# Performance work log

Measured on AMD Instinct MI355X. Metric: run time of the kernel, lower is better.

Reference implementation:

```python
import jax, jax.numpy as jnp
from jax import lax
import numpy as np

B, L, FEAT, EXTRA, K1 = 128, 128, 36, 12, 3
EMB, H, A, T_OUT = 6, 1024, 256, 24
CONV_OUT = FEAT - 2 * (K1 - 1)  # 32


def _conv1d(x, w):
    return lax.conv_general_dilated(x, w, (1,), 'VALID', dimension_numbers=('NCW', 'OIW', 'NCW'))


def _lstm(x_t, h, c, Wih, Whh, b):
    g = x_t @ Wih.T + h @ Whh.T + b
    i, f, gg, o = jnp.split(g, 4, axis=-1)
    c = jax.nn.sigmoid(f) * c + jax.nn.sigmoid(i) * jnp.tanh(gg)
    h = jax.nn.sigmoid(o) * jnp.tanh(c)
    return h, c


def setup_inputs():
    key = jax.random.key(0)
    ks = jax.random.split(key, 20)
    s = 0.05
    r = lambda k, sh: jax.random.normal(k, sh, jnp.float32) * s
    return {
        'x': jax.random.normal(ks[0], (B, L, FEAT + EXTRA), jnp.float32),
        'conv1_w': r(ks[1], (L, L, K1)), 'conv1_b': r(ks[2], (L,)),
        'conv2_w': r(ks[3], (L, L, K1)), 'conv2_b': r(ks[4], (L,)),
        'lin3_w': r(ks[5], (EMB, CONV_OUT)), 'lin3_b': r(ks[6], (EMB,)),
        'enc_Wih': r(ks[7], (4 * H, EMB + EXTRA)), 'enc_Whh': r(ks[8], (4 * H, H)), 'enc_b': r(ks[9], (4 * H,)),
        'attn_Wq': r(ks[10], (A, H)), 'attn_Wk': r(ks[11], (A, H)), 'attn_Wv': r(ks[12], (1, A)),
        'dec_Wih': r(ks[13], (4 * H, 2 * H)), 'dec_Whh': r(ks[14], (4 * H, H)), 'dec_b': r(ks[15], (4 * H,)),
        'out_w': r(ks[16], (1, H)), 'out_b': r(ks[17], (1,)),
    }


def reference(x, conv1_w, conv1_b, conv2_w, conv2_b, lin3_w, lin3_b,
              enc_Wih, enc_Whh, enc_b, attn_Wq, attn_Wk, attn_Wv,
              dec_Wih, dec_Whh, dec_b, out_w, out_b):
    # CNN feature extractor over the dense (short-interval) features
    dense = x[:, :, :FEAT]                                   # (B, L, 36)
    h1 = jax.nn.softplus(_conv1d(dense, conv1_w) + conv1_b[None, :, None])
    h2 = jax.nn.relu(_conv1d(h1, conv2_w) + conv2_b[None, :, None])  # (B, L, 32)
    lin = jnp.einsum('blf,ef->ble', h2, lin3_w) + lin3_b     # (B, L, EMB)
    lstm_in = jnp.concatenate([lin, x[:, :, FEAT:]], axis=2)  # (B, L, EMB+EXTRA)

    # LSTM encoder
    def enc_step(carry, xt):
        h, c = carry
        h, c = _lstm(xt, h, c, enc_Wih, enc_Whh, enc_b)
        return (h, c), h
    z = jnp.zeros((B, H), jnp.float32)
    (h, c), outs = lax.scan(enc_step, (z, z), lstm_in.transpose(1, 0, 2))
    enc_out = outs.transpose(1, 0, 2)                        # (B, L, H)
    s = enc_out[:, -1]

    # fixed-size key buffer; original appends s_t each step (lengths 128..151)
    M = L - 1 + T_OUT
    buf0 = jnp.zeros((B, M, H), jnp.float32).at[:, :L - 1].set(enc_out[:, :-1])
    pos = jnp.arange(M)

    def dec_step(carry, t):
        h, c, s, buf = carry
        buf = lax.dynamic_update_slice(buf, s[:, None, :], (0, L - 1 + t, 0))
        mask = (pos <= L - 1 + t).astype(buf.dtype)
        q = jnp.stack([h, c], axis=1)                        # (B, 2, H)
        qp = q @ attn_Wq.T                                   # (B, 2, A)
        kp = buf @ attn_Wk.T                                 # (B, M, A)
        feats = jnp.tanh(qp[:, :, None, :] + kp[:, None, :, :])  # (B, 2, M, A)
        scores = jnp.einsum('bnma,a->bnm', feats, attn_Wv[0])
        # original: softmax over dim=1 (query axis); mask keys post-softmax
        w = jax.nn.softmax(scores, axis=1) * mask[None, None, :]
        ctx = jnp.einsum('bnm,bmh->bnh', w, buf).reshape(B, 2 * H)
        h, c = _lstm(ctx, h, c, dec_Wih, dec_Whh, dec_b)
        y = (h @ out_w.T + out_b)[:, 0]
        return (h, c, h, buf), y

    _, ys = lax.scan(dec_step, (h, c, s, buf0), jnp.arange(T_OUT))
    return ys.T                                              # (B, T_OUT)
```

## Files before the change

kernel.cpp:

```cpp
#include <hip/hip_runtime.h>
#include <math.h>


#define NB 128
#define NL 128
#define NH 1024
#define NA 256
#define NT 24
#define NM 151

typedef __attribute__((ext_vector_type(8))) short bf16x8;
typedef __attribute__((ext_vector_type(8))) short s16x8;
typedef __attribute__((ext_vector_type(4))) float f32x4;

#define MFMA(a, b, acc) __builtin_amdgcn_mfma_f32_16x16x32_bf16(a, b, acc, 0, 0, 0)

#define I16_SCALE 32767.0f
#define I16_INV   (1.0f / 32767.0f)

__device__ __forceinline__ float sig_f(float x) {
  return 1.0f / (1.0f + __expf(-x));
}
__device__ __forceinline__ float tanh_f(float x) {
  x = fminf(9.0f, fmaxf(-9.0f, x));
  float e = __expf(2.0f * x);
  return (e - 1.0f) / (e + 1.0f);
}
__device__ __forceinline__ unsigned short f2bf(float f) {
  unsigned int u = __float_as_uint(f);
  u = (u + 0x7FFFu + ((u >> 16) & 1u)) >> 16;
  return (unsigned short)u;
}
__device__ __forceinline__ float bf2f(unsigned short u) {
  return __uint_as_float(((unsigned int)u) << 16);
}
__device__ __forceinline__ short f2i16(float f) {
  return (short)__float2int_rn(f * I16_SCALE);
}

__global__ __launch_bounds__(128) void conv_front(
    const float* __restrict__ x,
    const float* __restrict__ w1, const float* __restrict__ b1,
    const float* __restrict__ w2, const float* __restrict__ b2,
    const float* __restrict__ w3, const float* __restrict__ b3,
    float* __restrict__ lstm_in)
{
  int b = blockIdx.x;
  int t = threadIdx.x;
  __shared__ float d[128][36];
  __shared__ float h1[128][34];
  __shared__ float h2[128][32];

  const float* xr = x + (size_t)(b * NL + t) * 48;
  #pragma unroll
  for (int f = 0; f < 36; ++f) d[t][f] = xr[f];
  __syncthreads();

  float acc[34];
  {
    float bias = b1[t];
    #pragma unroll
    for (int w = 0; w < 34; ++w) acc[w] = bias;
  }
  const float* wr = w1 + t * 384;
  for (int ci = 0; ci < 128; ++ci) {
    float row[36];
    #pragma unroll
    for (int f = 0; f < 36; ++f) row[f] = d[ci][f];
    float wa = wr[ci * 3 + 0], wb = wr[ci * 3 + 1], wc = wr[ci * 3 + 2];
    #pragma unroll
    for (int w = 0; w < 34; ++w)
      acc[w] += row[w] * wa + row[w + 1] * wb + row[w + 2] * wc;
  }
  #pragma unroll
  for (int w = 0; w < 34; ++w) {
    float z = acc[w];
    h1[t][w] = (z > 20.0f) ? z : log1pf(__expf(z));
  }
  __syncthreads();

  float acc2[32];
  {
    float bias = b2[t];
    #pragma unroll
    for (int w = 0; w < 32; ++w) acc2[w] = bias;
  }
  const float* wr2 = w2 + t * 384;
  for (int ci = 0; ci < 128; ++ci) {
    float row[34];
    #pragma unroll
    for (int f = 0; f < 34; ++f) row[f] = h1[ci][f];
    float wa = wr2[ci * 3 + 0], wb = wr2[ci * 3 + 1], wc = wr2[ci * 3 + 2];
    #pragma unroll
    for (int w = 0; w < 32; ++w)
      acc2[w] += row[w] * wa + row[w + 1] * wb + row[w + 2] * wc;
  }
  #pragma unroll
  for (int w = 0; w < 32; ++w) h2[t][w] = fmaxf(acc2[w], 0.0f);
  __syncthreads();

  float* outr = lstm_in + (size_t)(b * NL + t) * 18;
  #pragma unroll
  for (int e = 0; e < 6; ++e) {
    float s = b3[e];
    #pragma unroll
    for (int f = 0; f < 32; ++f) s += h2[t][f] * w3[e * 32 + f];
    outr[e] = s;
  }
  #pragma unroll
  for (int j = 0; j < 12; ++j) outr[6 + j] = xr[36 + j];
}

__global__ void frag_w4(const float* __restrict__ src, int K, int kshift,
                        unsigned short* __restrict__ hi,
                        unsigned short* __restrict__ lo, int ngroups)
{
  int o = blockIdx.x * 256 + threadIdx.x;
  if (o >= ngroups) return;
  int lane = o & 63;
  int ki = (o >> 6) & ((1 << kshift) - 1);
  int t2 = o >> (6 + kshift);
  int l15 = lane & 15, q = lane >> 4;
  int grow = (l15 >> 2) * 1024 + t2 * 4 + (l15 & 3);
  const float* s = src + (size_t)grow * K + ki * 32 + q * 8;
  unsigned short hv[8], lv[8];
  #pragma unroll
  for (int j = 0; j < 8; ++j) {
    float v = s[j];
    hv[j] = f2bf(v);
    lv[j] = f2bf(v - bf2f(hv[j]));
  }
  size_t e = (size_t)o * 8;
  *(ushort4*)(hi + e) = make_ushort4(hv[0], hv[1], hv[2], hv[3]);
  *(ushort4*)(hi + e + 4) = make_ushort4(hv[4], hv[5], hv[6], hv[7]);
  *(ushort4*)(lo + e) = make_ushort4(lv[0], lv[1], lv[2], lv[3]);
  *(ushort4*)(lo + e + 4) = make_ushort4(lv[4], lv[5], lv[6], lv[7]);
}

__global__ void frag_wqk(const float* __restrict__ wq,
                         const float* __restrict__ wk,
                         unsigned short* __restrict__ hi,
                         unsigned short* __restrict__ lo)
{
  int o = blockIdx.x * 256 + threadIdx.x;
  if (o >= 65536) return;
  int lane = o & 63;
  int ki = (o >> 6) & 31;
  int ntile = o >> 11;
  int l15 = lane & 15, q = lane >> 4;
  int row = ntile * 16 + l15;
  int k = ki * 32 + q * 8;
  const float* s = (row < 256) ? (wq + (size_t)row * 1024 + k)
                               : (wk + (size_t)(row - 256) * 1024 + k);
  unsigned short hv[8], lv[8];
  #pragma unroll
  for (int j = 0; j < 8; ++j) {
    float v = s[j];
    hv[j] = f2bf(v);
    lv[j] = f2bf(v - bf2f(hv[j]));
  }
  size_t e = (size_t)o * 8;
  *(ushort4*)(hi + e) = make_ushort4(hv[0], hv[1], hv[2], hv[3]);
  *(ushort4*)(hi + e + 4) = make_ushort4(hv[4], hv[5], hv[6], hv[7]);
  *(ushort4*)(lo + e) = make_ushort4(lv[0], lv[1], lv[2], lv[3]);
  *(ushort4*)(lo + e + 4) = make_ushort4(lv[4], lv[5], lv[6], lv[7]);
}

__global__ void frag_wx4(const float* __restrict__ wih,
                         unsigned short* __restrict__ hi,
                         unsigned short* __restrict__ lo)
{
  int o = blockIdx.x * 256 + threadIdx.x;
  if (o >= 16384) return;
  int lane = o & 63;
  int t2 = o >> 6;
  int l15 = lane & 15, q = lane >> 4;
  int grow = (l15 >> 2) * 1024 + t2 * 4 + (l15 & 3);
  unsigned short hv[8], lv[8];
  #pragma unroll
  for (int j = 0; j < 8; ++j) {
    int k = q * 8 + j;
    float v = (k < 18) ? wih[(size_t)grow * 18 + k] : 0.0f;
    hv[j] = f2bf(v);
    lv[j] = f2bf(v - bf2f(hv[j]));
  }
  size_t e = (size_t)o * 8;
  *(ushort4*)(hi + e) = make_ushort4(hv[0], hv[1], hv[2], hv[3]);
  *(ushort4*)(hi + e + 4) = make_ushort4(hv[4], hv[5], hv[6], hv[7]);
  *(ushort4*)(lo + e) = make_ushort4(lv[0], lv[1], lv[2], lv[3]);
  *(ushort4*)(lo + e + 4) = make_ushort4(lv[4], lv[5], lv[6], lv[7]);
}

__global__ void frag_xs(const float* __restrict__ lstm_in,
                        unsigned short* __restrict__ hi,
                        unsigned short* __restrict__ lo)
{
  int o = blockIdx.x * 256 + threadIdx.x;
  if (o >= 65536) return;
  int lane = o & 63;
  int btile = (o >> 6) & 7;
  int t = o >> 9;
  int l15 = lane & 15, q = lane >> 4;
  int b = btile * 16 + l15;
  unsigned short hv[8], lv[8];
  #pragma unroll
  for (int j = 0; j < 8; ++j) {
    int k = q * 8 + j;
    float v = (k < 18) ? lstm_in[(size_t)(b * NL + t) * 18 + k] : 0.0f;
    hv[j] = f2bf(v);
    lv[j] = f2bf(v - bf2f(hv[j]));
  }
  size_t e = (size_t)o * 8;
  *(ushort4*)(hi + e) = make_ushort4(hv[0], hv[1], hv[2], hv[3]);
  *(ushort4*)(hi + e + 4) = make_ushort4(hv[4], hv[5], hv[6], hv[7]);
  *(ushort4*)(lo + e) = make_ushort4(lv[0], lv[1], lv[2], lv[3]);
  *(ushort4*)(lo + e + 4) = make_ushort4(lv[4], lv[5], lv[6], lv[7]);
}

__global__ void init_all(float* __restrict__ c,
                         unsigned short* __restrict__ hhi0,
                         unsigned short* __restrict__ hlo0,
                         float* __restrict__ out) {
  int i = blockIdx.x * 256 + threadIdx.x;
  if (i < NB * NH) { c[i] = 0.0f; hhi0[i] = 0; hlo0[i] = 0; }
  if (i < NB * NT) out[i] = 0.0f;
}

__global__ __launch_bounds__(512) void enc_step(
    const unsigned short* __restrict__ hfi_hi,
    const unsigned short* __restrict__ hfi_lo,
    unsigned short* __restrict__ hfo_hi,
    unsigned short* __restrict__ hfo_lo,
    const unsigned short* __restrict__ Wf_hi,
    const unsigned short* __restrict__ Wf_lo,
    const unsigned short* __restrict__ Wxf_hi,
    const unsigned short* __restrict__ Wxf_lo,
    const unsigned short* __restrict__ xsf_hi,
    const unsigned short* __restrict__ xsf_lo,
    const float* __restrict__ encb,
    float* __restrict__ c,
    short* __restrict__ buf,
    int t)
{
  __shared__ float G[2][128][17];
  int tid = threadIdx.x;
  int w8 = tid >> 6, lane = tid & 63;
  int grp = w8 >> 2, wm = w8 & 3;
  int l15 = lane & 15, q4 = (lane >> 4) * 4;
  int bx = blockIdx.x;

  const unsigned short* Bh = Wf_hi + (size_t)bx * 16384 + lane * 8;
  const unsigned short* Bl = Wf_lo + (size_t)bx * 16384 + lane * 8;
  const unsigned short* A0h = hfi_hi + (size_t)(2 * wm) * 512 + lane * 8;
  const unsigned short* A1h = hfi_hi + (size_t)(2 * wm + 1) * 512 + lane * 8;
  const unsigned short* A0l = hfi_lo + (size_t)(2 * wm) * 512 + lane * 8;
  const unsigned short* A1l = hfi_lo + (size_t)(2 * wm + 1) * 512 + lane * 8;

  f32x4 a00 = {0,0,0,0}, a10 = {0,0,0,0};
  for (int i = 0; i < 16; ++i) {
    int ki = grp * 16 + i;
    size_t ao = (size_t)ki * 4096;
    size_t bo = (size_t)ki * 512;
    bf16x8 x0h = *(const bf16x8*)(A0h + ao);
    bf16x8 x0l = *(const bf16x8*)(A0l + ao);
    bf16x8 x1h = *(const bf16x8*)(A1h + ao);
    bf16x8 x1l = *(const bf16x8*)(A1l + ao);
    bf16x8 yh = *(const bf16x8*)(Bh + bo);
    bf16x8 yl = *(const bf16x8*)(Bl + bo);
    a00 = MFMA(x0h, yh, a00); a00 = MFMA(x0l, yh, a00); a00 = MFMA(x0h, yl, a00);
    a10 = MFMA(x1h, yh, a10); a10 = MFMA(x1l, yh, a10); a10 = MFMA(x1h, yl, a10);
  }
  if (grp == 0) {
    size_t xo0 = ((size_t)t * 8 + 2 * wm) * 512 + lane * 8;
    size_t xo1 = xo0 + 512;
    bf16x8 x0h = *(const bf16x8*)(xsf_hi + xo0);
    bf16x8 x0l = *(const bf16x8*)(xsf_lo + xo0);
    bf16x8 x1h = *(const bf16x8*)(xsf_hi + xo1);
    bf16x8 x1l = *(const bf16x8*)(xsf_lo + xo1);
    size_t wo = (size_t)bx * 512 + lane * 8;
    bf16x8 yh = *(const bf16x8*)(Wxf_hi + wo);
    bf16x8 yl = *(const bf16x8*)(Wxf_lo + wo);
    a00 = MFMA(x0h, yh, a00); a00 = MFMA(x0l, yh, a00); a00 = MFMA(x0h, yl, a00);
    a10 = MFMA(x1h, yh, a10); a10 = MFMA(x1l, yh, a10); a10 = MFMA(x1h, yl, a10);
  }
  #pragma unroll
  for (int r = 0; r < 4; ++r) {
    G[grp][32 * wm + q4 + r][l15]      = a00[r];
    G[grp][32 * wm + 16 + q4 + r][l15] = a10[r];
  }
  __syncthreads();

  if (tid < 128) {
    int b = tid;
    int kc = bx * 4;
    float4 cold = *(const float4*)(c + (size_t)b * NH + kc);
    float rc[4], rh[4];
    #pragma unroll
    for (int j = 0; j < 4; ++j) {
      float gate[4];
      #pragma unroll
      for (int q = 0; q < 4; ++q) {
        int gi = q * 4 + j;
        gate[q] = G[0][b][gi] + G[1][b][gi] + encb[q * NH + kc + j];
      }
      float co = (&cold.x)[j];
      float cn = sig_f(gate[1]) * co + sig_f(gate[0]) * tanh_f(gate[2]);
      float hn = sig_f(gate[3]) * tanh_f(cn);
      rc[j] = cn; rh[j] = hn;
    }
    *(float4*)(c + (size_t)b * NH + kc) = make_float4(rc[0], rc[1], rc[2], rc[3]);
    unsigned short hh[4], hl[4];
    short hq[4];
    #pragma unroll
    for (int j = 0; j < 4; ++j) {
      hh[j] = f2bf(rh[j]);
      hl[j] = f2bf(rh[j] - bf2f(hh[j]));
      hq[j] = f2i16(rh[j]);
    }
    int ki = kc >> 5, qq = (kc >> 3) & 3, j8 = kc & 7;
    size_t fo = (size_t)ki * 4096 + (b >> 4) * 512 + ((b & 15) + 16 * qq) * 8 + j8;
    *(ushort4*)(hfo_hi + fo) = make_ushort4(hh[0], hh[1], hh[2], hh[3]);
    *(ushort4*)(hfo_lo + fo) = make_ushort4(hl[0], hl[1], hl[2], hl[3]);
    *(short4*)(buf + (size_t)(b * NM + t) * NH + kc) =
        make_short4(hq[0], hq[1], hq[2], hq[3]);
  }
}

__global__ __launch_bounds__(256) void dec_prep(
    const unsigned short* __restrict__ hf_hi,
    const unsigned short* __restrict__ hf_lo,
    const float* __restrict__ c,
    unsigned short* __restrict__ qhi, unsigned short* __restrict__ qlo)
{
  int b = blockIdx.x;
  int j4 = threadIdx.x * 4;
  int ki = j4 >> 5, qq = (j4 >> 3) & 3, j8 = j4 & 7;
  size_t fh = (size_t)ki * 4096 + (b >> 4) * 512 + ((b & 15) + 16 * qq) * 8 + j8;
  ushort4 hv = *(const ushort4*)(hf_hi + fh);
  ushort4 lv = *(const ushort4*)(hf_lo + fh);
  float4 cv = *(const float4*)(c + (size_t)b * NH + j4);
  unsigned short ch[4], cl[4];
  float cf[4] = {cv.x, cv.y, cv.z, cv.w};
  #pragma unroll
  for (int k = 0; k < 4; ++k) {
    ch[k] = f2bf(cf[k]); cl[k] = f2bf(cf[k] - bf2f(ch[k]));
  }
  int rt = (2 * b) >> 4;
  int rl = ((2 * b) & 15) + 16 * qq;
  size_t fq = (size_t)ki * 8192 + rt * 512 + rl * 8 + j8;
  *(ushort4*)(qhi + fq) = hv;
  *(ushort4*)(qlo + fq) = lv;
  *(ushort4*)(qhi + fq + 8) = make_ushort4(ch[0], ch[1], ch[2], ch[3]);
  *(ushort4*)(qlo + fq + 8) = make_ushort4(cl[0], cl[1], cl[2], cl[3]);
}

__global__ __launch_bounds__(128) void gemm_qk(
    const unsigned short* __restrict__ Ahi, const unsigned short* __restrict__ Alo,
    const unsigned short* __restrict__ Bhi, const unsigned short* __restrict__ Blo,
    float* __restrict__ C)
{
  int tid = threadIdx.x;
  int w = tid >> 6, lane = tid & 63;
  int l15 = lane & 15, q4 = (lane >> 4) * 4;
  int mtile = blockIdx.x;
  int ntile = blockIdx.y * 2 + w;

  const unsigned short* Ah = Ahi + (size_t)mtile * 512 + lane * 8;
  const unsigned short* Al = Alo + (size_t)mtile * 512 + lane * 8;
  const unsigned short* Bh = Bhi + (size_t)ntile * 16384 + lane * 8;
  const unsigned short* Bl = Blo + (size_t)ntile * 16384 + lane * 8;
  f32x4 acc = {0, 0, 0, 0};
  for (int ki = 0; ki < 32; ++ki) {
    size_t ao = (size_t)ki * 8192;
    size_t bo = (size_t)ki * 512;
    bf16x8 ah = *(const bf16x8*)(Ah + ao);
    bf16x8 al = *(const bf16x8*)(Al + ao);
    bf16x8 bh = *(const bf16x8*)(Bh + bo);
    bf16x8 bl = *(const bf16x8*)(Bl + bo);
    acc = MFMA(ah, bh, acc);
    acc = MFMA(al, bh, acc);
    acc = MFMA(ah, bl, acc);
  }
  #pragma unroll
  for (int r = 0; r < 4; ++r)
    C[(size_t)(mtile * 16 + q4 + r) * 512 + ntile * 16 + l15] = acc[r];
}

__global__ __launch_bounds__(256) void gemm_kp(
    const short* __restrict__ A,
    const unsigned short* __restrict__ Bhi,
    const unsigned short* __restrict__ Blo,
    unsigned short* __restrict__ C)
{
  int tid = threadIdx.x;
  int w = tid >> 6, lane = tid & 63;
  int l15 = lane & 15, q8 = (lane >> 4) * 8, q4 = (lane >> 4) * 4;
  size_t m0 = (size_t)blockIdx.x * 64;
  int n0 = blockIdx.y * 64 + w * 16;
  int ntile = 16 + blockIdx.y * 4 + w;

  const unsigned short* Bh = Bhi + (size_t)ntile * 16384 + lane * 8;
  const unsigned short* Bl = Blo + (size_t)ntile * 16384 + lane * 8;
  f32x4 acc[4] = {{0,0,0,0},{0,0,0,0},{0,0,0,0},{0,0,0,0}};
  for (int ki = 0; ki < 32; ++ki) {
    int ko = ki * 32 + q8;
    size_t bo = (size_t)ki * 512;
    bf16x8 bh = *(const bf16x8*)(Bh + bo);
    bf16x8 bl = *(const bf16x8*)(Bl + bo);
    #pragma unroll
    for (int i = 0; i < 4; ++i) {
      s16x8 av = *(const s16x8*)(A + (m0 + 16 * i + l15) * (size_t)NH + ko);
      bf16x8 ah;
      #pragma unroll
      for (int k = 0; k < 8; ++k)
        ah[k] = (short)f2bf((float)av[k] * I16_INV);
      acc[i] = MFMA(ah, bh, acc[i]);
      acc[i] = MFMA(ah, bl, acc[i]);
    }
  }
  #pragma unroll
  for (int i = 0; i < 4; ++i)
    #pragma unroll
    for (int r = 0; r < 4; ++r)
      C[(m0 + 16 * i + q4 + r) * NA + n0 + l15] = f2bf(acc[i][r]);
}

__global__ __launch_bounds__(256) void attn_kernel(
    const float* __restrict__ qkout,
    unsigned short* __restrict__ kp,
    const short* __restrict__ buf,
    const float* __restrict__ Wv,
    unsigned short* __restrict__ Xfhi,
    unsigned short* __restrict__ Xflo,
    int t)
{
  int b = blockIdx.x;
  int tid = threadIdx.x;
  int Mt = NL + t;
  __shared__ float sWv[256], q0[256], q1[256], kNew[256];
  __shared__ float sc[2][NM + 1];
  __shared__ float w0s[NM + 1], w1s[NM + 1];
  sWv[tid] = Wv[tid];
  q0[tid] = qkout[(size_t)(2 * b) * 512 + tid];
  q1[tid] = qkout[(size_t)(2 * b + 1) * 512 + tid];
  float kn = qkout[(size_t)(2 * b) * 512 + 256 + tid];
  kNew[tid] = kn;
  kp[((size_t)(b * NM) + (NL - 1 + t)) * NA + tid] = f2bf(kn);
  __syncthreads();

  for (int idx = tid; idx < 2 * Mt; idx += 256) {
    int m = idx >> 1, n = idx & 1;
    const float* q = n ? q1 : q0;
    float s = 0.0f;
    if (m == Mt - 1) {
      for (int a = 0; a < NA; ++a) s += tanh_f(q[a] + kNew[a]) * sWv[a];
    } else {
      const unsigned short* kpr = kp + ((size_t)(b * NM) + m) * NA;
      for (int a = 0; a < NA; a += 4) {
        ushort4 kv = *(const ushort4*)(kpr + a);
        s += tanh_f(q[a + 0] + bf2f(kv.x)) * sWv[a + 0];
        s += tanh_f(q[a + 1] + bf2f(kv.y)) * sWv[a + 1];
        s += tanh_f(q[a + 2] + bf2f(kv.z)) * sWv[a + 2];
        s += tanh_f(q[a + 3] + bf2f(kv.w)) * sWv[a + 3];
      }
    }
    sc[n][m] = s;
  }
  __syncthreads();
  for (int m = tid; m < Mt; m += 256) {
    float s0 = sc[0][m], s1 = sc[1][m];
    float mx = fmaxf(s0, s1);
    float e0 = __expf(s0 - mx), e1 = __expf(s1 - mx);
    float inv = 1.0f / (e0 + e1);
    w0s[m] = e0 * inv;
    w1s[m] = e1 * inv;
  }
  __syncthreads();

  float4 a0 = {0, 0, 0, 0}, a1 = {0, 0, 0, 0};
  const short* bb = buf + ((size_t)b * NM) * NH + tid * 4;
  for (int m = 0; m < Mt; ++m) {
    short4 v = *(const short4*)(bb + (size_t)m * NH);
    float vx = (float)v.x * I16_INV, vy = (float)v.y * I16_INV;
    float vz = (float)v.z * I16_INV, vw = (float)v.w * I16_INV;
    float w0 = w0s[m], w1 = w1s[m];
    a0.x += vx * w0; a0.y += vy * w0; a0.z += vz * w0; a0.w += vw * w0;
    a1.x += vx * w1; a1.y += vy * w1; a1.z += vz * w1; a1.w += vw * w1;
  }
  float v0[4] = {a0.x, a0.y, a0.z, a0.w};
  float v1[4] = {a1.x, a1.y, a1.z, a1.w};
  unsigned short h0[4], l0[4], h1v[4], l1v[4];
  #pragma unroll
  for (int k = 0; k < 4; ++k) {
    h0[k] = f2bf(v0[k]); l0[k] = f2bf(v0[k] - bf2f(h0[k]));
    h1v[k] = f2bf(v1[k]); l1v[k] = f2bf(v1[k] - bf2f(h1v[k]));
  }
  int k0 = tid * 4;
  size_t fo0 = (size_t)(k0 >> 5) * 4096 + (b >> 4) * 512 +
               ((b & 15) + 16 * ((k0 >> 3) & 3)) * 8 + (k0 & 7);
  int k1 = 1024 + tid * 4;
  size_t fo1 = (size_t)(k1 >> 5) * 4096 + (b >> 4) * 512 +
               ((b & 15) + 16 * ((k1 >> 3) & 3)) * 8 + (k1 & 7);
  *(ushort4*)(Xfhi + fo0) = make_ushort4(h0[0], h0[1], h0[2], h0[3]);
  *(ushort4*)(Xflo + fo0) = make_ushort4(l0[0], l0[1], l0[2], l0[3]);
  *(ushort4*)(Xfhi + fo1) = make_ushort4(h1v[0], h1v[1], h1v[2], h1v[3]);
  *(ushort4*)(Xflo + fo1) = make_ushort4(l1v[0], l1v[1], l1v[2], l1v[3]);
}

__global__ __launch_bounds__(512) void dec_step(
    const unsigned short* __restrict__ Xfhi,
    const unsigned short* __restrict__ Xflo,
    const unsigned short* __restrict__ qin_hi,
    const unsigned short* __restrict__ qin_lo,
    unsigned short* __restrict__ qout_hi,
    unsigned short* __restrict__ qout_lo,
    const unsigned short* __restrict__ Wdxf_hi,
    const unsigned short* __restrict__ Wdxf_lo,
    const unsigned short* __restrict__ Wdhf_hi,
    const unsigned short* __restrict__ Wdhf_lo,
    const float* __restrict__ decb,
    float* __restrict__ c,
    short* __restrict__ buf,
    const float* __restrict__ out_w, const float* __restrict__ out_b,
    float* __restrict__ out, int t)
{
  __shared__ float G[2][128][17];
  int tid = threadIdx.x;
  int w8 = tid >> 6, lane = tid & 63;
  int grp = w8 >> 2, wm = w8 & 3;
  int l15 = lane & 15, q4 = (lane >> 4) * 4;
  int bx = blockIdx.x;

  f32x4 a00 = {0,0,0,0}, a10 = {0,0,0,0};

  {
    const unsigned short* Wh = Wdxf_hi + (size_t)bx * 32768 + lane * 8;
    const unsigned short* Wl = Wdxf_lo + (size_t)bx * 32768 + lane * 8;
    const unsigned short* X0h = Xfhi + (size_t)(2 * wm) * 512 + lane * 8;
    const unsigned short* X1h = Xfhi + (size_t)(2 * wm + 1) * 512 + lane * 8;
    const unsigned short* X0l = Xflo + (size_t)(2 * wm) * 512 + lane * 8;
    const unsigned short* X1l = Xflo + (size_t)(2 * wm + 1) * 512 + lane * 8;
    int klo = grp ? 48 : 0;
    int khi = grp ? 64 : 48;
    for (int ki = klo; ki < khi; ++ki) {
      size_t ao = (size_t)ki * 4096;
      size_t bo = (size_t)ki * 512;
      bf16x8 x0h = *(const bf16x8*)(X0h + ao);
      bf16x8 x0l = *(const bf16x8*)(X0l + ao);
      bf16x8 x1h = *(const bf16x8*)(X1h + ao);
      bf16x8 x1l = *(const bf16x8*)(X1l + ao);
      bf16x8 yh = *(const bf16x8*)(Wh + bo);
      bf16x8 yl = *(const bf16x8*)(Wl + bo);
      a00 = MFMA(x0h, yh, a00); a00 = MFMA(x0l, yh, a00); a00 = MFMA(x0h, yl, a00);
      a10 = MFMA(x1h, yh, a10); a10 = MFMA(x1l, yh, a10); a10 = MFMA(x1h, yl, a10);
    }
  }
  if (grp) {
    int qt0 = 4 * wm + (l15 >> 3);
    int ln = 2 * (l15 & 7) + 16 * (lane >> 4);
    const unsigned short* A0h = qin_hi + (size_t)qt0 * 512 + ln * 8;
    const unsigned short* A0l = qin_lo + (size_t)qt0 * 512 + ln * 8;
    const unsigned short* A1h = qin_hi + (size_t)(qt0 + 2) * 512 + ln * 8;
    const unsigned short* A1l = qin_lo + (size_t)(qt0 + 2) * 512 + ln * 8;
    const unsigned short* Bh = Wdhf_hi + (size_t)bx * 16384 + lane * 8;
    const unsigned short* Bl = Wdhf_lo + (size_t)bx * 16384 + lane * 8;
    for (int ki = 0; ki < 32; ++ki) {
      size_t ao = (size_t)ki * 8192;
      size_t bo = (size_t)ki * 512;
      bf16x8 x0h = *(const bf16x8*)(A0h + ao);
      bf16x8 x0l = *(const bf16x8*)(A0l + ao);
      bf16x8 x1h = *(const bf16x8*)(A1h + ao);
      bf16x8 x1l = *(const bf16x8*)(A1l + ao);
      bf16x8 yh = *(const bf16x8*)(Bh + bo);
      bf16x8 yl = *(const bf16x8*)(Bl + bo);
      a00 = MFMA(x0h, yh, a00); a00 = MFMA(x0l, yh, a00); a00 = MFMA(x0h, yl, a00);
      a10 = MFMA(x1h, yh, a10); a10 = MFMA(x1l, yh, a10); a10 = MFMA(x1h, yl, a10);
    }
  }
  #pragma unroll
  for (int r = 0; r < 4; ++r) {
    G[grp][32 * wm + q4 + r][l15]      = a00[r];
    G[grp][32 * wm + 16 + q4 + r][l15] = a10[r];
  }
  __syncthreads();

  if (tid < 128) {
    int b = tid;
    int kc = bx * 4;
    float4 cold = *(const float4*)(c + (size_t)b * NH + kc);
    float rc[4], rh[4];
    #pragma unroll
    for (int j = 0; j < 4; ++j) {
      float gate[4];
      #pragma unroll
      for (int q = 0; q < 4; ++q) {
        int gi = q * 4 + j;
        gate[q] = G[0][b][gi] + G[1][b][gi] + decb[q * NH + kc + j];
      }
      float co = (&cold.x)[j];
      float cn = sig_f(gate[1]) * co + sig_f(gate[0]) * tanh_f(gate[2]);
      float hn = sig_f(gate[3]) * tanh_f(cn);
      rc[j] = cn; rh[j] = hn;
    }
    *(float4*)(c + (size_t)b * NH + kc) = make_float4(rc[0], rc[1], rc[2], rc[3]);

    float py = 0.0f;
    #pragma unroll
    for (int j = 0; j < 4; ++j) py += rh[j] * out_w[kc + j];
    if (bx == 0) py += out_b[0];
    atomicAdd(&out[b * NT + t], py);

    if (t < NT - 1) {
      unsigned short hh[4], hl[4], ch[4], cl[4];
      short hq[4];
      #pragma unroll
      for (int j = 0; j < 4; ++j) {
        hh[j] = f2bf(rh[j]); hl[j] = f2bf(rh[j] - bf2f(hh[j]));
        ch[j] = f2bf(rc[j]); cl[j] = f2bf(rc[j] - bf2f(ch[j]));
        hq[j] = f2i16(rh[j]);
      }
      *(short4*)(buf + (size_t)(b * NM + NL + t) * NH + kc) =
          make_short4(hq[0], hq[1], hq[2], hq[3]);
      int ki = kc >> 5, qq = (kc >> 3) & 3, j8 = kc & 7;
      int rt = (2 * b) >> 4;
      int rl = ((2 * b) & 15) + 16 * qq;
      size_t fq = (size_t)ki * 8192 + rt * 512 + rl * 8 + j8;
      *(ushort4*)(qout_hi + fq) = make_ushort4(hh[0], hh[1], hh[2], hh[3]);
      *(ushort4*)(qout_lo + fq) = make_ushort4(hl[0], hl[1], hl[2], hl[3]);
      *(ushort4*)(qout_hi + fq + 8) = make_ushort4(ch[0], ch[1], ch[2], ch[3]);
      *(ushort4*)(qout_lo + fq + 8) = make_ushort4(cl[0], cl[1], cl[2], cl[3]);
    }
  }
}

extern "C" void kernel_launch(void* const* d_in, const int* in_sizes, int n_in,
                              void* d_out, int out_size, void* d_ws, size_t ws_size,
                              hipStream_t stream) {
  const float* x       = (const float*)d_in[0];
  const float* conv1_w = (const float*)d_in[1];
  const float* conv1_b = (const float*)d_in[2];
  const float* conv2_w = (const float*)d_in[3];
  const float* conv2_b = (const float*)d_in[4];
  const float* lin3_w  = (const float*)d_in[5];
  const float* lin3_b  = (const float*)d_in[6];
  const float* enc_Wih = (const float*)d_in[7];
  const float* enc_Whh = (const float*)d_in[8];
  const float* enc_b   = (const float*)d_in[9];
  const float* attn_Wq = (const float*)d_in[10];
  const float* attn_Wk = (const float*)d_in[11];
  const float* attn_Wv = (const float*)d_in[12];
  const float* dec_Wih = (const float*)d_in[13];
  const float* dec_Whh = (const float*)d_in[14];
  const float* dec_b   = (const float*)d_in[15];
  const float* out_w   = (const float*)d_in[16];
  const float* out_b   = (const float*)d_in[17];
  float* out = (float*)d_out;

  unsigned short* W = (unsigned short*)d_ws;
  short*          buf    = (short*)W;
  unsigned short* kp     = W + (size_t)19791872;
  unsigned short* qA_hi  = kp + 4947968;
  unsigned short* qA_lo  = qA_hi + 262144;
  unsigned short* qB_hi  = qA_lo + 262144;
  unsigned short* qB_lo  = qB_hi + 262144;
  unsigned short* Xf_hi  = qB_lo + 262144;
  unsigned short* Xf_lo  = Xf_hi + 262144;
  unsigned short* Wqkf_hi = Xf_lo + 262144;
  unsigned short* Wqkf_lo = Wqkf_hi + 524288;
  unsigned short* Wdhf_hi = Wqkf_lo + 524288;
  unsigned short* Wdhf_lo = Wdhf_hi + 4194304;
  unsigned short* Wdxf_hi = Wdhf_lo + 4194304;
  unsigned short* Wdxf_lo = Wdxf_hi + 8388608;
  float* c     = (float*)(Wdxf_lo + 8388608);
  float* qkout = c + 131072;
  unsigned short* hfA_hi = Wdxf_hi;
  unsigned short* hfA_lo = Wdxf_hi + 131072;
  unsigned short* hfB_hi = Wdxf_hi + 262144;
  unsigned short* hfB_lo = Wdxf_hi + 393216;
  unsigned short* xsf_hi = Wdxf_hi + 524288;
  unsigned short* xsf_lo = xsf_hi + 524288;
  unsigned short* Wxf_hi = xsf_lo + 524288;
  unsigned short* Wxf_lo = Wxf_hi + 131072;
  float* lstm_in = (float*)Wdxf_lo;

  init_all<<<512, 256, 0, stream>>>(c, hfA_hi, hfA_lo, out);
  conv_front<<<NB, 128, 0, stream>>>(x, conv1_w, conv1_b, conv2_w, conv2_b,
                                     lin3_w, lin3_b, lstm_in);
  frag_xs<<<256, 256, 0, stream>>>(lstm_in, xsf_hi, xsf_lo);
  frag_wx4<<<64, 256, 0, stream>>>(enc_Wih, Wxf_hi, Wxf_lo);
  frag_w4<<<2048, 256, 0, stream>>>(enc_Whh, 1024, 5, Wdhf_hi, Wdhf_lo, 524288);
  frag_wqk<<<256, 256, 0, stream>>>(attn_Wq, attn_Wk, Wqkf_hi, Wqkf_lo);

  for (int t = 0; t < NL; ++t) {
    const unsigned short* ih = (t & 1) ? hfB_hi : hfA_hi;
    const unsigned short* il = (t & 1) ? hfB_lo : hfA_lo;
    unsigned short* oh = (t & 1) ? hfA_hi : hfB_hi;
    unsigned short* ol = (t & 1) ? hfA_lo : hfB_lo;
    enc_step<<<256, 512, 0, stream>>>(ih, il, oh, ol, Wdhf_hi, Wdhf_lo,
                                      Wxf_hi, Wxf_lo, xsf_hi, xsf_lo,
                                      enc_b, c, buf, t);
  }

  dec_prep<<<NB, 256, 0, stream>>>(hfA_hi, hfA_lo, c, qA_hi, qA_lo);
  gemm_kp<<<dim3(302, 4), 256, 0, stream>>>(buf, Wqkf_hi, Wqkf_lo, kp);

  frag_w4<<<4096, 256, 0, stream>>>(dec_Wih, 2048, 6, Wdxf_hi, Wdxf_lo, 1048576);
  frag_w4<<<2048, 256, 0, stream>>>(dec_Whh, 1024, 5, Wdhf_hi, Wdhf_lo, 524288);

  for (int t = 0; t < NT; ++t) {
    const unsigned short* qih = (t & 1) ? qB_hi : qA_hi;
    const unsigned short* qil = (t & 1) ? qB_lo : qA_lo;
    unsigned short* qoh = (t & 1) ? qA_hi : qB_hi;
    unsigned short* qol = (t & 1) ? qA_lo : qB_lo;
    gemm_qk<<<dim3(16, 16), 128, 0, stream>>>(qih, qil, Wqkf_hi, Wqkf_lo, qkout);
    attn_kernel<<<NB, 256, 0, stream>>>(qkout, kp, buf, attn_Wv, Xf_hi, Xf_lo, t);
    dec_step<<<256, 512, 0, stream>>>(Xf_hi, Xf_lo, qih, qil, qoh, qol,
                                      Wdxf_hi, Wdxf_lo, Wdhf_hi, Wdhf_lo,
                                      dec_b, c, buf, out_w, out_b, out, t);
  }
}
```

Measured before the change: 4.622 ms.

## Fuse encoder timesteps into one persistent cooperative kernel with grid barrier

```diff
diff --git a/kernel.cpp b/kernel.cpp
--- a/kernel.cpp
+++ b/kernel.cpp
@@ -8,6 +8,7 @@
 #define NA 256
 #define NT 24
 #define NM 151
+#define ENCB 64
 
 typedef __attribute__((ext_vector_type(8))) short bf16x8;
 typedef __attribute__((ext_vector_type(8))) short s16x8;
@@ -36,6 +37,51 @@
 }
 __device__ __forceinline__ short f2i16(float f) {
   return (short)__float2int_rn(f * I16_SCALE);
+}
+
+__device__ __forceinline__ bf16x8 ald16(const unsigned short* p) {
+  unsigned long long a = __hip_atomic_load((const unsigned long long*)p,
+      __ATOMIC_RELAXED, __HIP_MEMORY_SCOPE_AGENT);
+  unsigned long long b = __hip_atomic_load((const unsigned long long*)(p + 4),
+      __ATOMIC_RELAXED, __HIP_MEMORY_SCOPE_AGENT);
+  union { unsigned long long u[2]; bf16x8 v; } x;
+  x.u[0] = a; x.u[1] = b;
+  return x.v;
+}
+
+__device__ __forceinline__ void ast8(unsigned short* p, unsigned short a,
+                                     unsigned short b, unsigned short cc,
+                                     unsigned short d) {
+  unsigned long long u = (unsigned long long)a | ((unsigned long long)b << 16) |
+                         ((unsigned long long)cc << 32) |
+                         ((unsigned long long)d << 48);
+  __hip_atomic_store((unsigned long long*)p, u, __ATOMIC_RELAXED,
+                     __HIP_MEMORY_SCOPE_AGENT);
+}
+
+__device__ __forceinline__ void gbar(unsigned int* bar, unsigned int ep) {
+  __syncthreads();
+  if (blockIdx.x == 0) {
+    int tid = threadIdx.x;
+    if (tid > 0 && tid < ENCB) {
+      while (__hip_atomic_load(&bar[tid * 32], __ATOMIC_RELAXED,
+                               __HIP_MEMORY_SCOPE_AGENT) < ep)
+        __builtin_amdgcn_s_sleep(1);
+    }
+    __syncthreads();
+    if (tid == 0)
+      __hip_atomic_store(&bar[ENCB * 32], ep, __ATOMIC_RELAXED,
+                         __HIP_MEMORY_SCOPE_AGENT);
+  } else {
+    if (threadIdx.x == 0) {
+      __hip_atomic_store(&bar[blockIdx.x * 32], ep, __ATOMIC_RELAXED,
+                         __HIP_MEMORY_SCOPE_AGENT);
+      while (__hip_atomic_load(&bar[ENCB * 32], __ATOMIC_RELAXED,
+                               __HIP_MEMORY_SCOPE_AGENT) < ep)
+        __builtin_amdgcn_s_sleep(1);
+    }
+    __syncthreads();
+  }
 }
 
 __global__ __launch_bounds__(128) void conv_front(
@@ -220,17 +266,17 @@
 __global__ void init_all(float* __restrict__ c,
                          unsigned short* __restrict__ hhi0,
                          unsigned short* __restrict__ hlo0,
-                         float* __restrict__ out) {
+                         float* __restrict__ out,
+                         unsigned int* __restrict__ bar) {
   int i = blockIdx.x * 256 + threadIdx.x;
   if (i < NB * NH) { c[i] = 0.0f; hhi0[i] = 0; hlo0[i] = 0; }
   if (i < NB * NT) out[i] = 0.0f;
-}
-
-__global__ __launch_bounds__(512) void enc_step(
-    const unsigned short* __restrict__ hfi_hi,
-    const unsigned short* __restrict__ hfi_lo,
-    unsigned short* __restrict__ hfo_hi,
-    unsigned short* __restrict__ hfo_lo,
+  if (i < ENCB * 32 + 32) bar[i] = 0;
+}
+
+__global__ __launch_bounds__(512) void enc_all(
+    unsigned short* __restrict__ hfA_hi, unsigned short* __restrict__ hfA_lo,
+    unsigned short* __restrict__ hfB_hi, unsigned short* __restrict__ hfB_lo,
     const unsigned short* __restrict__ Wf_hi,
     const unsigned short* __restrict__ Wf_lo,
     const unsigned short* __restrict__ Wxf_hi,
@@ -240,90 +286,113 @@
     const float* __restrict__ encb,
     float* __restrict__ c,
     short* __restrict__ buf,
-    int t)
-{
-  __shared__ float G[2][128][17];
-  int tid = threadIdx.x;
+    unsigned int* __restrict__ bar)
+{
+  __shared__ float G[4][128][17];
+  int tid = threadIdx.x, bx = blockIdx.x;
   int w8 = tid >> 6, lane = tid & 63;
-  int grp = w8 >> 2, wm = w8 & 3;
   int l15 = lane & 15, q4 = (lane >> 4) * 4;
-  int bx = blockIdx.x;
-
-  const unsigned short* Bh = Wf_hi + (size_t)bx * 16384 + lane * 8;
-  const unsigned short* Bl = Wf_lo + (size_t)bx * 16384 + lane * 8;
-  const unsigned short* A0h = hfi_hi + (size_t)(2 * wm) * 512 + lane * 8;
-  const unsigned short* A1h = hfi_hi + (size_t)(2 * wm + 1) * 512 + lane * 8;
-  const unsigned short* A0l = hfi_lo + (size_t)(2 * wm) * 512 + lane * 8;
-  const unsigned short* A1l = hfi_lo + (size_t)(2 * wm + 1) * 512 + lane * 8;
-
-  f32x4 a00 = {0,0,0,0}, a10 = {0,0,0,0};
-  for (int i = 0; i < 16; ++i) {
-    int ki = grp * 16 + i;
-    size_t ao = (size_t)ki * 4096;
-    size_t bo = (size_t)ki * 512;
-    bf16x8 x0h = *(const bf16x8*)(A0h + ao);
-    bf16x8 x0l = *(const bf16x8*)(A0l + ao);
-    bf16x8 x1h = *(const bf16x8*)(A1h + ao);
-    bf16x8 x1l = *(const bf16x8*)(A1l + ao);
-    bf16x8 yh = *(const bf16x8*)(Bh + bo);
-    bf16x8 yl = *(const bf16x8*)(Bl + bo);
-    a00 = MFMA(x0h, yh, a00); a00 = MFMA(x0l, yh, a00); a00 = MFMA(x0h, yl, a00);
-    a10 = MFMA(x1h, yh, a10); a10 = MFMA(x1l, yh, a10); a10 = MFMA(x1h, yl, a10);
-  }
-  if (grp == 0) {
-    size_t xo0 = ((size_t)t * 8 + 2 * wm) * 512 + lane * 8;
-    size_t xo1 = xo0 + 512;
-    bf16x8 x0h = *(const bf16x8*)(xsf_hi + xo0);
-    bf16x8 x0l = *(const bf16x8*)(xsf_lo + xo0);
-    bf16x8 x1h = *(const bf16x8*)(xsf_hi + xo1);
-    bf16x8 x1l = *(const bf16x8*)(xsf_lo + xo1);
-    size_t wo = (size_t)bx * 512 + lane * 8;
-    bf16x8 yh = *(const bf16x8*)(Wxf_hi + wo);
-    bf16x8 yl = *(const bf16x8*)(Wxf_lo + wo);
-    a00 = MFMA(x0h, yh, a00); a00 = MFMA(x0l, yh, a00); a00 = MFMA(x0h, yl, a00);
-    a10 = MFMA(x1h, yh, a10); a10 = MFMA(x1l, yh, a10); a10 = MFMA(x1h, yl, a10);
-  }
-  #pragma unroll
-  for (int r = 0; r < 4; ++r) {
-    G[grp][32 * wm + q4 + r][l15]      = a00[r];
-    G[grp][32 * wm + 16 + q4 + r][l15] = a10[r];
-  }
-  __syncthreads();
-
-  if (tid < 128) {
-    int b = tid;
-    int kc = bx * 4;
-    float4 cold = *(const float4*)(c + (size_t)b * NH + kc);
-    float rc[4], rh[4];
-    #pragma unroll
-    for (int j = 0; j < 4; ++j) {
-      float gate[4];
+  int ab = w8;
+
+  const unsigned short* B0h = Wf_hi + (size_t)(bx * 4) * 16384 + lane * 8;
+  const unsigned short* B0l = Wf_lo + (size_t)(bx * 4) * 16384 + lane * 8;
+  const unsigned short* X0h = Wxf_hi + (size_t)(bx * 4) * 512 + lane * 8;
+  const unsigned short* X0l = Wxf_lo + (size_t)(bx * 4) * 512 + lane * 8;
+
+  int eb = tid & 127;
+  int ecg = tid >> 7;
+  int ekc = bx * 16 + ecg * 4;
+  float bias[4][4];
+  #pragma unroll
+  for (int q = 0; q < 4; ++q)
+    #pragma unroll
+    for (int j = 0; j < 4; ++j)
+      bias[q][j] = encb[q * NH + ekc + j];
+  float4 creg = make_float4(0.f, 0.f, 0.f, 0.f);
+  int eki = ekc >> 5, eqq = (ekc >> 3) & 3, ej8 = ekc & 7;
+  size_t efo = (size_t)eki * 4096 + (eb >> 4) * 512 +
+               ((eb & 15) + 16 * eqq) * 8 + ej8;
+
+  for (int t = 0; t < NL; ++t) {
+    const unsigned short* hih = (t & 1) ? hfB_hi : hfA_hi;
+    const unsigned short* hil = (t & 1) ? hfB_lo : hfA_lo;
+    unsigned short* hoh = (t & 1) ? hfA_hi : hfB_hi;
+    unsigned short* hol = (t & 1) ? hfA_lo : hfB_lo;
+
+    f32x4 a0 = {0,0,0,0}, a1 = {0,0,0,0}, a2 = {0,0,0,0}, a3 = {0,0,0,0};
+    for (int ki = 0; ki < 32; ++ki) {
+      size_t base = (size_t)ki * 4096 + ab * 512 + lane * 8;
+      bf16x8 xh = ald16(hih + base);
+      bf16x8 xl = ald16(hil + base);
+      size_t bo = (size_t)ki * 512;
+      bf16x8 y0h = *(const bf16x8*)(B0h + bo);
+      bf16x8 y0l = *(const bf16x8*)(B0l + bo);
+      bf16x8 y1h = *(const bf16x8*)(B0h + 16384 + bo);
+      bf16x8 y1l = *(const bf16x8*)(B0l + 16384 + bo);
+      bf16x8 y2h = *(const bf16x8*)(B0h + 32768 + bo);
+      bf16x8 y2l = *(const bf16x8*)(B0l + 32768 + bo);
+      bf16x8 y3h = *(const bf16x8*)(B0h + 49152 + bo);
+      bf16x8 y3l = *(const bf16x8*)(B0l + 49152 + bo);
+      a0 = MFMA(xh, y0h, a0); a0 = MFMA(xl, y0h, a0); a0 = MFMA(xh, y0l, a0);
+      a1 = MFMA(xh, y1h, a1); a1 = MFMA(xl, y1h, a1); a1 = MFMA(xh, y1l, a1);
+      a2 = MFMA(xh, y2h, a2); a2 = MFMA(xl, y2h, a2); a2 = MFMA(xh, y2l, a2);
+      a3 = MFMA(xh, y3h, a3); a3 = MFMA(xl, y3h, a3); a3 = MFMA(xh, y3l, a3);
+    }
+    {
+      size_t xo = ((size_t)t * 8 + ab) * 512 + lane * 8;
+      bf16x8 xh = *(const bf16x8*)(xsf_hi + xo);
+      bf16x8 xl = *(const bf16x8*)(xsf_lo + xo);
+      bf16x8 y0h = *(const bf16x8*)X0h;
+      bf16x8 y0l = *(const bf16x8*)X0l;
+      bf16x8 y1h = *(const bf16x8*)(X0h + 512);
+      bf16x8 y1l = *(const bf16x8*)(X0l + 512);
+      bf16x8 y2h = *(const bf16x8*)(X0h + 1024);
+      bf16x8 y2l = *(const bf16x8*)(X0l + 1024);
+      bf16x8 y3h = *(const bf16x8*)(X0h + 1536);
+      bf16x8 y3l = *(const bf16x8*)(X0l + 1536);
+      a0 = MFMA(xh, y0h, a0); a0 = MFMA(xl, y0h, a0); a0 = MFMA(xh, y0l, a0);
+      a1 = MFMA(xh, y1h, a1); a1 = MFMA(xl, y1h, a1); a1 = MFMA(xh, y1l, a1);
+      a2 = MFMA(xh, y2h, a2); a2 = MFMA(xl, y2h, a2); a2 = MFMA(xh, y2l, a2);
+      a3 = MFMA(xh, y3h, a3); a3 = MFMA(xl, y3h, a3); a3 = MFMA(xh, y3l, a3);
+    }
+    #pragma unroll
+    for (int r = 0; r < 4; ++r) {
+      G[0][ab * 16 + q4 + r][l15] = a0[r];
+      G[1][ab * 16 + q4 + r][l15] = a1[r];
+      G[2][ab * 16 + q4 + r][l15] = a2[r];
+      G[3][ab * 16 + q4 + r][l15] = a3[r];
+    }
+    __syncthreads();
+
+    {
+      float rh[4];
+      float* cp = &creg.x;
       #pragma unroll
-      for (int q = 0; q < 4; ++q) {
-        int gi = q * 4 + j;
-        gate[q] = G[0][b][gi] + G[1][b][gi] + encb[q * NH + kc + j];
+      for (int j = 0; j < 4; ++j) {
+        float gate[4];
+        #pragma unroll
+        for (int q = 0; q < 4; ++q)
+          gate[q] = G[ecg][eb][q * 4 + j] + bias[q][j];
+        float cn = sig_f(gate[1]) * cp[j] + sig_f(gate[0]) * tanh_f(gate[2]);
+        float hn = sig_f(gate[3]) * tanh_f(cn);
+        cp[j] = cn; rh[j] = hn;
       }
-      float co = (&cold.x)[j];
-      float cn = sig_f(gate[1]) * co + sig_f(gate[0]) * tanh_f(gate[2]);
-      float hn = sig_f(gate[3]) * tanh_f(cn);
-      rc[j] = cn; rh[j] = hn;
-    }
-    *(float4*)(c + (size_t)b * NH + kc) = make_float4(rc[0], rc[1], rc[2], rc[3]);
-    unsigned short hh[4], hl[4];
-    short hq[4];
-    #pragma unroll
-    for (int j = 0; j < 4; ++j) {
-      hh[j] = f2bf(rh[j]);
-      hl[j] = f2bf(rh[j] - bf2f(hh[j]));
-      hq[j] = f2i16(rh[j]);
-    }
-    int ki = kc >> 5, qq = (kc >> 3) & 3, j8 = kc & 7;
-    size_t fo = (size_t)ki * 4096 + (b >> 4) * 512 + ((b & 15) + 16 * qq) * 8 + j8;
-    *(ushort4*)(hfo_hi + fo) = make_ushort4(hh[0], hh[1], hh[2], hh[3]);
-    *(ushort4*)(hfo_lo + fo) = make_ushort4(hl[0], hl[1], hl[2], hl[3]);
-    *(short4*)(buf + (size_t)(b * NM + t) * NH + kc) =
-        make_short4(hq[0], hq[1], hq[2], hq[3]);
-  }
+      unsigned short hh[4], hl[4];
+      short hq[4];
+      #pragma unroll
+      for (int j = 0; j < 4; ++j) {
+        hh[j] = f2bf(rh[j]);
+        hl[j] = f2bf(rh[j] - bf2f(hh[j]));
+        hq[j] = f2i16(rh[j]);
+      }
+      ast8(hoh + efo, hh[0], hh[1], hh[2], hh[3]);
+      ast8(hol + efo, hl[0], hl[1], hl[2], hl[3]);
+      *(short4*)(buf + (size_t)(eb * NM + t) * NH + ekc) =
+          make_short4(hq[0], hq[1], hq[2], hq[3]);
+    }
+    if (t < NL - 1) gbar(bar, (unsigned int)(t + 1));
+  }
+  *(float4*)(c + (size_t)eb * NH + ekc) = creg;
 }
 
 __global__ __launch_bounds__(256) void dec_prep(
@@ -682,8 +751,9 @@
   unsigned short* Wxf_hi = xsf_lo + 524288;
   unsigned short* Wxf_lo = Wxf_hi + 131072;
   float* lstm_in = (float*)Wdxf_lo;
-
-  init_all<<<512, 256, 0, stream>>>(c, hfA_hi, hfA_lo, out);
+  unsigned int* bar = (unsigned int*)(Wdxf_lo + 1048576);
+
+  init_all<<<512, 256, 0, stream>>>(c, hfA_hi, hfA_lo, out, bar);
   conv_front<<<NB, 128, 0, stream>>>(x, conv1_w, conv1_b, conv2_w, conv2_b,
                                      lin3_w, lin3_b, lstm_in);
   frag_xs<<<256, 256, 0, stream>>>(lstm_in, xsf_hi, xsf_lo);
@@ -691,14 +761,15 @@
   frag_w4<<<2048, 256, 0, stream>>>(enc_Whh, 1024, 5, Wdhf_hi, Wdhf_lo, 524288);
   frag_wqk<<<256, 256, 0, stream>>>(attn_Wq, attn_Wk, Wqkf_hi, Wqkf_lo);
 
-  for (int t = 0; t < NL; ++t) {
-    const unsigned short* ih = (t & 1) ? hfB_hi : hfA_hi;
-    const unsigned short* il = (t & 1) ? hfB_lo : hfA_lo;
-    unsigned short* oh = (t & 1) ? hfA_hi : hfB_hi;
-    unsigned short* ol = (t & 1) ? hfA_lo : hfB_lo;
-    enc_step<<<256, 512, 0, stream>>>(ih, il, oh, ol, Wdhf_hi, Wdhf_lo,
-                                      Wxf_hi, Wxf_lo, xsf_hi, xsf_lo,
-                                      enc_b, c, buf, t);
+  {
+    void* ea[] = {
+      (void*)&hfA_hi, (void*)&hfA_lo, (void*)&hfB_hi, (void*)&hfB_lo,
+      (void*)&Wdhf_hi, (void*)&Wdhf_lo, (void*)&Wxf_hi, (void*)&Wxf_lo,
+      (void*)&xsf_hi, (void*)&xsf_lo, (void*)&enc_b, (void*)&c, (void*)&buf,
+      (void*)&bar
+    };
+    hipLaunchCooperativeKernel((void*)enc_all, dim3(ENCB), dim3(512), ea, 0,
+                               stream);
   }
 
   dec_prep<<<NB, 256, 0, stream>>>(hfA_hi, hfA_lo, c, qA_hi, qA_lo);
```

Result: slower. 7.411 ms (+60.3%).
